# Kernel tuning notes

Measured on AMD Instinct MI355X. Metric: run time of the kernel, lower is better.

Reference implementation:

```python
import jax, jax.numpy as jnp
import numpy as np

GRID_SIZE = 8
SPLINE_ORDER = 3
GRID_LO, GRID_HI = -1.0, 1.0
EPS = 1e-5  # InstanceNorm2d default eps
C = 16
K = GRID_SIZE + SPLINE_ORDER  # number of B-spline basis channels per input channel


def make_grid():
    h = (GRID_HI - GRID_LO) / GRID_SIZE
    # extended knot vector, length grid_size + 2*spline_order + 1
    return jnp.arange(-SPLINE_ORDER, GRID_SIZE + SPLINE_ORDER + 1, dtype=jnp.float32) * h + GRID_LO


def bspline_bases(x, grid):
    # x: [B,C,H,W] -> bases: [B,C,H,W,K] via Cox-de Boor recursion
    xu = x[..., None]
    bases = ((xu >= grid[:-1]) & (xu < grid[1:])).astype(x.dtype)
    for k in range(1, SPLINE_ORDER + 1):
        left = grid[:-(k + 1)]
        right = grid[k:-1]
        delta = jnp.where(right == left, jnp.ones_like(right), right - left)
        bases = ((xu - left) / delta) * bases[..., :-1] + \
                ((grid[k + 1:] - xu) / (grid[k + 1:] - grid[1:-k])) * bases[..., 1:]
    return bases


def conv2d(x, w):
    # NCHW conv, stride 1, padding 1 (kernel 3x3), bias=False as in KANConv2DLayer
    return jax.lax.conv_general_dilated(
        x, w, window_strides=(1, 1), padding=[(1, 1), (1, 1)],
        dimension_numbers=('NCHW', 'OIHW', 'NCHW'))


def instance_norm(x):
    # nn.InstanceNorm2d(affine=False): normalize over H,W per (N,C)
    m = jnp.mean(x, axis=(2, 3), keepdims=True)
    v = jnp.var(x, axis=(2, 3), keepdims=True)
    return (x - m) * jax.lax.rsqrt(v + EPS)


def prelu(x, a):
    return jnp.where(x >= 0, x, a * x)


def kan_conv_layer(x, base_w, spline_w, prelu_a, grid):
    base_out = conv2d(jax.nn.silu(x), base_w)
    b = bspline_bases(x, grid)                      # [B,C,H,W,K]
    B, Cx, H, W, Kx = b.shape
    b = jnp.moveaxis(b, -1, 2).reshape(B, Cx * Kx, H, W)
    spline_out = conv2d(b, spline_w)
    return prelu(instance_norm(base_out + spline_out), prelu_a)


def setup_inputs() -> dict:
    key = jax.random.key(0)
    ks = jax.random.split(key, 5)
    s = 0.05
    return {
        'x': jax.random.normal(ks[0], (4, C, 512, 512), jnp.float32),
        'base_w1': jax.random.normal(ks[1], (C, C, 3, 3), jnp.float32) * s,
        'spline_w1': jax.random.normal(ks[2], (C, C * K, 3, 3), jnp.float32) * s,
        'prelu_a1': jnp.float32(0.25),
        'base_w2': jax.random.normal(ks[3], (C, C, 3, 3), jnp.float32) * s,
        'spline_w2': jax.random.normal(ks[4], (C, C * K, 3, 3), jnp.float32) * s,
        'prelu_a2': jnp.float32(0.25),
    }


def reference(x, base_w1, spline_w1, prelu_a1, base_w2, spline_w2, prelu_a2):
    grid = make_grid()
    y = kan_conv_layer(x, base_w1, spline_w1, prelu_a1, grid)
    y = kan_conv_layer(y, base_w2, spline_w2, prelu_a2, grid)
    return jax.nn.sigmoid(y)
```

## Files before the change

kernel.cpp:

```cpp
#include <hip/hip_runtime.h>
#include <cstddef>
#include <cstdint>

#define HW    512
#define CCH   16
#define TR    12
#define HTILE 18
#define NPIX2 252
#define NSLOT 12

typedef _Float16 f16x8 __attribute__((ext_vector_type(8)));
typedef float    f32x4 __attribute__((ext_vector_type(4)));

__device__ __forceinline__ float h2f(ushort u) {
    _Float16 h = __builtin_bit_cast(_Float16, u);
    return (float)h;
}
__device__ __forceinline__ ushort f2h(float f) {
    _Float16 h = (_Float16)f;
    return __builtin_bit_cast(ushort, h);
}
__device__ __forceinline__ uint pack2h(float a, float b) {
    return (uint)f2h(a) | ((uint)f2h(b) << 16);
}

__device__ __forceinline__ void derived12(float x, uint* u) {
    float si = x / (1.0f + __expf(-x));
    float t  = fmaf(x, 4.0f, 7.0f);
    t = fminf(fmaxf(t, -1.0f), 15.0f);
    float ft = floorf(t);
    int   ci = (int)ft;
    float uu = t - ft;
    float um = 1.0f - uu;
    float u2 = uu * uu, m2 = um * um;
    float u3 = u2 * uu, m3 = m2 * um;
    const float c16 = 0.16666667f, c23 = 0.66666667f;
    float w0 = u3 * c16;
    float w3 = m3 * c16;
    float w2 = fmaf(0.5f, u3, c23 - u2);
    float w1 = fmaf(0.5f, m3, c23 - m2);
    uint64_t P = (uint64_t)f2h(w3)
               | ((uint64_t)f2h(w2) << 16)
               | ((uint64_t)f2h(w1) << 32)
               | ((uint64_t)f2h(w0) << 48);
    int s = 16 * ci - 48;
    int d = s >> 6;
    int e = s & 63;
    uint64_t Q = P << e;
    uint64_t R = (P >> (63 - e)) >> 1;
    uint64_t O0 = (d == 0) ? Q : (d == -1) ? R : 0ull;
    uint64_t O1 = (d == 1) ? Q : (d ==  0) ? R : 0ull;
    uint64_t O2 = (d == 2) ? Q : (d ==  1) ? R : 0ull;
    O2 = (O2 & 0x0000ffffffffffffull) | ((uint64_t)f2h(si) << 48);
    u[0] = (uint)O0; u[1] = (uint)(O0 >> 32);
    u[2] = (uint)O1; u[3] = (uint)(O1 >> 32);
    u[4] = (uint)O2; u[5] = (uint)(O2 >> 32);
}

__global__ void __launch_bounds__(64) prep_w(
    const float* __restrict__ bw1, const float* __restrict__ sw1,
    const float* __restrict__ bw2, const float* __restrict__ sw2,
    uint4* __restrict__ wtab1, uint4* __restrict__ wtab2,
    float* __restrict__ part1, float* __restrict__ part2)
{
    const int s    = blockIdx.x;
    const int lane = threadIdx.x;
    const float* bw; const float* sw; uint4* wt;
    if (blockIdx.y == 0) { bw = bw1; sw = sw1; wt = wtab1; }
    else                 { bw = bw2; sw = sw2; wt = wtab2; }

    if (s == 0) {
        float* p = (blockIdx.y == 0) ? part1 : part2;
        p[lane] = 0.0f;
        p[64 + lane] = 0.0f;
    }

    const int co = lane & 15, q = lane >> 4;
    const int chunk = s / 27, sl = s - chunk * 27;
    uint u[4];
#pragma unroll
    for (int jj = 0; jj < 4; ++jj) {
        float w[2];
#pragma unroll
        for (int h = 0; h < 2; ++h) {
            int j   = jj * 2 + h;
            int kl  = 32 * sl + 8 * q + j;
            int tap = kl / 96;
            int r   = kl - tap * 96;
            int ci  = r / 12;
            int kv  = r - ci * 12;
            int cin = chunk * 8 + ci;
            w[h] = (kv == 11) ? bw[(co * 16 + cin) * 9 + tap]
                              : sw[(co * 176 + cin * 11 + kv) * 9 + tap];
        }
        u[jj] = pack2h(w[0], w[1]);
    }
    wt[s * 64 + lane] = make_uint4(u[0], u[1], u[2], u[3]);
}

template<bool IN_H, bool OUT_H, bool NORM_IN>
__global__ __launch_bounds__(256, 2) void conv_mfma(
    const void* __restrict__ in_v,
    const uint4* __restrict__ wtab,
    void* __restrict__ out_v,
    const float* __restrict__ stats_in,
    const float* __restrict__ a_in,
    float* __restrict__ part_out)
{
    __shared__ uint4 dt16[NSLOT * NPIX2];
    __shared__ float sn[32];

    const int tid  = threadIdx.x;
    const int lane = tid & 63;
    const int wv   = tid >> 6;
    const int m    = lane & 15;
    const int q    = lane >> 4;
    const int bx0  = blockIdx.x * 16;
    const int by0  = blockIdx.y * TR;
    const int b    = blockIdx.z;

    const float*  inf = (const float*)in_v;
    const ushort* inh = (const ushort*)in_v;

    float pa = 0.0f;
    if (NORM_IN) {
        pa = *a_in;
        if (tid < 32) sn[tid] = stats_in[b * 32 + tid];
    }

    f32x4 acc[3];
#pragma unroll
    for (int t = 0; t < 3; ++t) acc[t] = f32x4{0.f, 0.f, 0.f, 0.f};

#pragma unroll 1
    for (int chunk = 0; chunk < 2; ++chunk) {
        __syncthreads();

        float v0[4], v1[4];
        uint  bofs[4], cps[4];
        bool  live[4];
#pragma unroll
        for (int k = 0; k < 4; ++k) {
            int it  = tid + k * 256;
            bool lv = (it < NPIX2 * 4);
            int cp  = it & 3;
            int pix = it >> 2;
            if (!lv) pix = 0;
            int py  = pix / HTILE;
            int px  = pix - py * HTILE;
            int gy  = by0 + py - 1;
            int gx  = bx0 + px - 1;
            bool ok = lv && ((unsigned)gy < (unsigned)HW)
                         && ((unsigned)gx < (unsigned)HW);
            live[k] = lv;
            cps[k]  = (uint)cp;
            bofs[k] = (uint)(cp * 3 * NPIX2 + pix);
            float a = -1.0e9f, c = -1.0e9f;
            if (ok) {
                size_t base = ((size_t)(b * CCH + chunk * 8 + cp * 2) << 18)
                            + ((size_t)gy << 9) + gx;
                if (IN_H) { a = h2f(inh[base]); c = h2f(inh[base + (1u << 18)]); }
                else      { a = inf[base];      c = inf[base + (1u << 18)]; }
            }
            v0[k] = a; v1[k] = c;
        }

        uint4 wf[27];
#pragma unroll
        for (int s = 0; s < 27; ++s) wf[s] = wtab[(chunk * 27 + s) * 64 + lane];

#pragma unroll
        for (int k = 0; k < 4; ++k) {
            if (live[k]) {
                float a0 = v0[k], c0 = v1[k];
                if (NORM_IN) {
                    int ci2 = (chunk * 8 + (int)cps[k] * 2) * 2;
                    a0 = (a0 - sn[ci2])     * sn[ci2 + 1];
                    a0 = (a0 >= 0.f) ? a0 : pa * a0;
                    c0 = (c0 - sn[ci2 + 2]) * sn[ci2 + 3];
                    c0 = (c0 >= 0.f) ? c0 : pa * c0;
                }
                uint uA[6], uB[6];
                derived12(a0, uA);
                derived12(c0, uB);
                uint bo = bofs[k];
                dt16[bo]             = make_uint4(uA[0], uA[1], uA[2], uA[3]);
                dt16[bo + NPIX2]     = make_uint4(uA[4], uA[5], uB[0], uB[1]);
                dt16[bo + 2 * NPIX2] = make_uint4(uB[2], uB[3], uB[4], uB[5]);
            }
        }
        __syncthreads();

        const uint pixbase = (uint)(wv * 3 * HTILE + m);
#pragma unroll
        for (int j = 0; j < 3; ++j) {
            const uint slotoff = (uint)((j * 4 + q) * NPIX2) + pixbase;
#pragma unroll
            for (int tdx = 0; tdx < 3; ++tdx) {
                f16x8 brow[5];
#pragma unroll
                for (int r6 = 0; r6 < 5; ++r6)
                    brow[r6] = *reinterpret_cast<const f16x8*>(
                        &dt16[slotoff + (uint)(r6 * HTILE + tdx)]);
#pragma unroll
                for (int tdy = 0; tdy < 3; ++tdy) {
                    const int s = (tdy * 3 + tdx) * 3 + j;
#pragma unroll
                    for (int t = 0; t < 3; ++t) {
                        acc[t] = __builtin_amdgcn_mfma_f32_16x16x32_f16(
                            __builtin_bit_cast(f16x8, wf[s]), brow[t + tdy],
                            acc[t], 0, 0, 0);
                    }
                }
            }
        }
    }

#pragma unroll
    for (int t = 0; t < 3; ++t) {
        int oy = by0 + wv * 3 + t;
        if (oy < HW) {
#pragma unroll
            for (int r = 0; r < 4; ++r) {
                int co = q * 4 + r;
                size_t idx = ((size_t)(b * CCH + co) << 18)
                           + ((size_t)oy << 9) + (bx0 + m);
                if (OUT_H) ((ushort*)out_v)[idx] = f2h(acc[t][r]);
                else       ((float*)out_v)[idx]  = acc[t][r];
            }
        }
    }

    float s4[4], q4[4];
#pragma unroll
    for (int r = 0; r < 4; ++r) { s4[r] = 0.0f; q4[r] = 0.0f; }
#pragma unroll
    for (int t = 0; t < 3; ++t) {
        int oy = by0 + wv * 3 + t;
        if (oy < HW) {
#pragma unroll
            for (int r = 0; r < 4; ++r) {
                s4[r] += acc[t][r];
                q4[r] = fmaf(acc[t][r], acc[t][r], q4[r]);
            }
        }
    }
#pragma unroll
    for (int off = 8; off > 0; off >>= 1) {
#pragma unroll
        for (int r = 0; r < 4; ++r) {
            s4[r] += __shfl_xor(s4[r], off);
            q4[r] += __shfl_xor(q4[r], off);
        }
    }
    __syncthreads();
    float* scr = (float*)dt16;
    if (m == 0) {
#pragma unroll
        for (int r = 0; r < 4; ++r) {
            scr[(wv * 16 + q * 4 + r) * 2 + 0] = s4[r];
            scr[(wv * 16 + q * 4 + r) * 2 + 1] = q4[r];
        }
    }
    __syncthreads();
    if (tid < 32) {
        int co = tid >> 1, which = tid & 1;
        float v = scr[(0 * 16 + co) * 2 + which] + scr[(1 * 16 + co) * 2 + which]
                + scr[(2 * 16 + co) * 2 + which] + scr[(3 * 16 + co) * 2 + which];
        atomicAdd(&part_out[(size_t)(b * CCH + co) * 2 + which], v);
    }
}

__global__ void __launch_bounds__(64) reduce_final(
    const float* __restrict__ part, float* __restrict__ stats)
{
    const int bc = threadIdx.x;
    const float inv = 1.0f / 262144.0f;
    float s  = part[bc * 2];
    float qq = part[bc * 2 + 1];
    float mval = s * inv;
    float var  = qq * inv - mval * mval;
    stats[bc * 2]     = mval;
    stats[bc * 2 + 1] = rsqrtf(var + 1e-5f);
}

__global__ void __launch_bounds__(256) final_sigmoid(
    float* __restrict__ out, const float* __restrict__ stats,
    const float* __restrict__ a_ptr)
{
    const float a = *a_ptr;
    const int i4 = blockIdx.x * 256 + threadIdx.x;
    const int bc = i4 >> 16;
    const float mm = stats[bc * 2];
    const float rr = stats[bc * 2 + 1];
    float4 v = reinterpret_cast<float4*>(out)[i4];
    float t;
    t = (v.x - mm) * rr; t = (t >= 0.f) ? t : a * t; v.x = 1.0f / (1.0f + __expf(-t));
    t = (v.y - mm) * rr; t = (t >= 0.f) ? t : a * t; v.y = 1.0f / (1.0f + __expf(-t));
    t = (v.z - mm) * rr; t = (t >= 0.f) ? t : a * t; v.z = 1.0f / (1.0f + __expf(-t));
    t = (v.w - mm) * rr; t = (t >= 0.f) ? t : a * t; v.w = 1.0f / (1.0f + __expf(-t));
    reinterpret_cast<float4*>(out)[i4] = v;
}

extern "C" void kernel_launch(void* const* d_in, const int* in_sizes, int n_in,
                              void* d_out, int out_size, void* d_ws, size_t ws_size,
                              hipStream_t stream)
{
    const float* x        = (const float*)d_in[0];
    const float* base_w1  = (const float*)d_in[1];
    const float* spline_w1= (const float*)d_in[2];
    const float* prelu_a1 = (const float*)d_in[3];
    const float* base_w2  = (const float*)d_in[4];
    const float* spline_w2= (const float*)d_in[5];
    const float* prelu_a2 = (const float*)d_in[6];
    float* out_f = (float*)d_out;
    char*  wsb   = (char*)d_ws;

    ushort* z1h    = (ushort*)wsb;
    uint4*  wtab1  = (uint4*)(wsb + 33554432);
    uint4*  wtab2  = (uint4*)(wsb + 33609728);
    float*  part1  = (float*)(wsb + 33665024);
    float*  part2  = (float*)(wsb + 33665536);
    float*  stats1 = (float*)(wsb + 33666048);
    float*  stats2 = (float*)(wsb + 33666560);

    dim3 cgrid(HW / 16, (HW + TR - 1) / TR, 4);
    dim3 cblk(256);

    prep_w<<<dim3(54, 2), 64, 0, stream>>>(base_w1, spline_w1, base_w2, spline_w2,
                                           wtab1, wtab2, part1, part2);

    conv_mfma<false, true, false><<<cgrid, cblk, 0, stream>>>(
        x, wtab1, z1h, nullptr, nullptr, part1);
    reduce_final<<<1, 64, 0, stream>>>(part1, stats1);

    conv_mfma<true, false, true><<<cgrid, cblk, 0, stream>>>(
        z1h, wtab2, out_f, stats1, prelu_a1, part2);
    reduce_final<<<1, 64, 0, stream>>>(part2, stats2);

    final_sigmoid<<<16384, cblk, 0, stream>>>(out_f, stats2, prelu_a2);
}
```

Before: 385.6 us.

## Warp-specialize conv kernel into producer/consumer halves with double-buffered LDS staging

The conv block grows to 512 threads. Four producer waves compute the B-spline/SiLU fp16 features into one of two LDS buffers while four consumer waves run MFMA on the other buffer. Each block now covers two 16-wide column tiles in sequence, and the row stride is padded from 252 to 254 entries, which may reduce LDS bank conflicts. This is meant to overlap feature generation with matrix math. In exchange it doubles LDS use, which may lower occupancy, and adds block-wide barriers between stages.

```diff
diff --git a/kernel.cpp b/kernel.cpp
--- a/kernel.cpp
+++ b/kernel.cpp
@@ -6,8 +6,11 @@
 #define CCH   16
 #define TR    12
 #define HTILE 18
-#define NPIX2 252
+#define HTR   14
+#define NPIXR 252
+#define NPIXP 254
 #define NSLOT 12
+#define BUFU  (NSLOT * NPIXP)
 
 typedef _Float16 f16x8 __attribute__((ext_vector_type(8)));
 typedef float    f32x4 __attribute__((ext_vector_type(4)));
@@ -99,7 +102,7 @@
 }
 
 template<bool IN_H, bool OUT_H, bool NORM_IN>
-__global__ __launch_bounds__(256, 2) void conv_mfma(
+__global__ __launch_bounds__(512, 2) void conv_mfma(
     const void* __restrict__ in_v,
     const uint4* __restrict__ wtab,
     void* __restrict__ out_v,
@@ -107,101 +110,97 @@
     const float* __restrict__ a_in,
     float* __restrict__ part_out)
 {
-    __shared__ uint4 dt16[NSLOT * NPIX2];
-    __shared__ float sn[32];
+    __shared__ uint4 dt16[2][BUFU];
+    __shared__ float scr[128];
 
     const int tid  = threadIdx.x;
+    const bool isC = tid < 256;
     const int lane = tid & 63;
-    const int wv   = tid >> 6;
+    const int wv   = (tid >> 6) & 3;
     const int m    = lane & 15;
     const int q    = lane >> 4;
-    const int bx0  = blockIdx.x * 16;
+    const int ptid = tid & 255;
     const int by0  = blockIdx.y * TR;
+    const int bxA  = blockIdx.x * 32;
+    const int bxB  = bxA + 16;
     const int b    = blockIdx.z;
 
     const float*  inf = (const float*)in_v;
     const ushort* inh = (const ushort*)in_v;
 
     float pa = 0.0f;
-    if (NORM_IN) {
-        pa = *a_in;
-        if (tid < 32) sn[tid] = stats_in[b * 32 + tid];
-    }
+    if (NORM_IN && !isC) pa = *a_in;
 
     f32x4 acc[3];
-#pragma unroll
-    for (int t = 0; t < 3; ++t) acc[t] = f32x4{0.f, 0.f, 0.f, 0.f};
-
-#pragma unroll 1
-    for (int chunk = 0; chunk < 2; ++chunk) {
-        __syncthreads();
-
+
+    auto stage = [&](int bx0t, int c, uint4* __restrict__ buf) {
         float v0[4], v1[4];
-        uint  bofs[4], cps[4];
+        float4 nm[4];
+        uint  bo4[4];
         bool  live[4];
 #pragma unroll
         for (int k = 0; k < 4; ++k) {
-            int it  = tid + k * 256;
-            bool lv = (it < NPIX2 * 4);
+            int it  = ptid + k * 256;
+            bool lv = (it < NPIXR * 4);
             int cp  = it & 3;
             int pix = it >> 2;
             if (!lv) pix = 0;
             int py  = pix / HTILE;
             int px  = pix - py * HTILE;
             int gy  = by0 + py - 1;
-            int gx  = bx0 + px - 1;
+            int gx  = bx0t + px - 1;
             bool ok = lv && ((unsigned)gy < (unsigned)HW)
                          && ((unsigned)gx < (unsigned)HW);
             live[k] = lv;
-            cps[k]  = (uint)cp;
-            bofs[k] = (uint)(cp * 3 * NPIX2 + pix);
-            float a = -1.0e9f, c = -1.0e9f;
+            bo4[k]  = (uint)(cp * 3 * NPIXP + pix);
+            float a = -1.0e9f, cc = -1.0e9f;
             if (ok) {
-                size_t base = ((size_t)(b * CCH + chunk * 8 + cp * 2) << 18)
+                size_t base = ((size_t)(b * CCH + c * 8 + cp * 2) << 18)
                             + ((size_t)gy << 9) + gx;
-                if (IN_H) { a = h2f(inh[base]); c = h2f(inh[base + (1u << 18)]); }
-                else      { a = inf[base];      c = inf[base + (1u << 18)]; }
-            }
-            v0[k] = a; v1[k] = c;
-        }
-
-        uint4 wf[27];
-#pragma unroll
-        for (int s = 0; s < 27; ++s) wf[s] = wtab[(chunk * 27 + s) * 64 + lane];
-
+                if (IN_H) { a = h2f(inh[base]); cc = h2f(inh[base + (1u << 18)]); }
+                else      { a = inf[base];      cc = inf[base + (1u << 18)]; }
+            }
+            if (NORM_IN && lv)
+                nm[k] = *reinterpret_cast<const float4*>(
+                    &stats_in[b * 32 + (c * 8 + cp * 2) * 2]);
+            v0[k] = a; v1[k] = cc;
+        }
 #pragma unroll
         for (int k = 0; k < 4; ++k) {
             if (live[k]) {
                 float a0 = v0[k], c0 = v1[k];
                 if (NORM_IN) {
-                    int ci2 = (chunk * 8 + (int)cps[k] * 2) * 2;
-                    a0 = (a0 - sn[ci2])     * sn[ci2 + 1];
+                    a0 = (a0 - nm[k].x) * nm[k].y;
                     a0 = (a0 >= 0.f) ? a0 : pa * a0;
-                    c0 = (c0 - sn[ci2 + 2]) * sn[ci2 + 3];
+                    c0 = (c0 - nm[k].z) * nm[k].w;
                     c0 = (c0 >= 0.f) ? c0 : pa * c0;
                 }
                 uint uA[6], uB[6];
                 derived12(a0, uA);
                 derived12(c0, uB);
-                uint bo = bofs[k];
-                dt16[bo]             = make_uint4(uA[0], uA[1], uA[2], uA[3]);
-                dt16[bo + NPIX2]     = make_uint4(uA[4], uA[5], uB[0], uB[1]);
-                dt16[bo + 2 * NPIX2] = make_uint4(uB[2], uB[3], uB[4], uB[5]);
-            }
-        }
-        __syncthreads();
-
+                uint bo = bo4[k];
+                buf[bo]             = make_uint4(uA[0], uA[1], uA[2], uA[3]);
+                buf[bo + NPIXP]     = make_uint4(uA[4], uA[5], uB[0], uB[1]);
+                buf[bo + 2 * NPIXP] = make_uint4(uB[2], uB[3], uB[4], uB[5]);
+            }
+        }
+    };
+
+    auto krun = [&](int c, const uint4* __restrict__ buf) {
+        uint4 wf[27];
+#pragma unroll
+        for (int s = 0; s < 27; ++s) wf[s] = wtab[(c * 27 + s) * 64 + lane];
         const uint pixbase = (uint)(wv * 3 * HTILE + m);
 #pragma unroll
         for (int j = 0; j < 3; ++j) {
-            const uint slotoff = (uint)((j * 4 + q) * NPIX2) + pixbase;
+            const uint slotoff = (uint)((j * 4 + q) * NPIXP) + pixbase;
 #pragma unroll
             for (int tdx = 0; tdx < 3; ++tdx) {
                 f16x8 brow[5];
 #pragma unroll
                 for (int r6 = 0; r6 < 5; ++r6)
                     brow[r6] = *reinterpret_cast<const f16x8*>(
-                        &dt16[slotoff + (uint)(r6 * HTILE + tdx)]);
+                        &buf[slotoff + (uint)(r6 * HTILE + tdx)]);
 #pragma unroll
                 for (int tdy = 0; tdy < 3; ++tdy) {
                     const int s = (tdy * 3 + tdx) * 3 + j;
@@ -214,61 +213,83 @@
                 }
             }
         }
-    }
-
-#pragma unroll
-    for (int t = 0; t < 3; ++t) {
-        int oy = by0 + wv * 3 + t;
-        if (oy < HW) {
+    };
+
+    auto epi1 = [&](int bx0t) {
+#pragma unroll
+        for (int t = 0; t < 3; ++t) {
+            int oy = by0 + wv * 3 + t;
+            if (oy < HW) {
+#pragma unroll
+                for (int r = 0; r < 4; ++r) {
+                    int co = q * 4 + r;
+                    size_t idx = ((size_t)(b * CCH + co) << 18)
+                               + ((size_t)oy << 9) + (bx0t + m);
+                    if (OUT_H) ((ushort*)out_v)[idx] = f2h(acc[t][r]);
+                    else       ((float*)out_v)[idx]  = acc[t][r];
+                }
+            }
+        }
+        float s4[4], q4[4];
+#pragma unroll
+        for (int r = 0; r < 4; ++r) { s4[r] = 0.0f; q4[r] = 0.0f; }
+#pragma unroll
+        for (int t = 0; t < 3; ++t) {
+            int oy = by0 + wv * 3 + t;
+            if (oy < HW) {
+#pragma unroll
+                for (int r = 0; r < 4; ++r) {
+                    s4[r] += acc[t][r];
+                    q4[r] = fmaf(acc[t][r], acc[t][r], q4[r]);
+                }
+            }
+        }
+#pragma unroll
+        for (int off = 8; off > 0; off >>= 1) {
 #pragma unroll
             for (int r = 0; r < 4; ++r) {
-                int co = q * 4 + r;
-                size_t idx = ((size_t)(b * CCH + co) << 18)
-                           + ((size_t)oy << 9) + (bx0 + m);
-                if (OUT_H) ((ushort*)out_v)[idx] = f2h(acc[t][r]);
-                else       ((float*)out_v)[idx]  = acc[t][r];
-            }
-        }
-    }
-
-    float s4[4], q4[4];
-#pragma unroll
-    for (int r = 0; r < 4; ++r) { s4[r] = 0.0f; q4[r] = 0.0f; }
-#pragma unroll
-    for (int t = 0; t < 3; ++t) {
-        int oy = by0 + wv * 3 + t;
-        if (oy < HW) {
+                s4[r] += __shfl_xor(s4[r], off);
+                q4[r] += __shfl_xor(q4[r], off);
+            }
+        }
+        if (m == 0) {
 #pragma unroll
             for (int r = 0; r < 4; ++r) {
-                s4[r] += acc[t][r];
-                q4[r] = fmaf(acc[t][r], acc[t][r], q4[r]);
-            }
-        }
-    }
-#pragma unroll
-    for (int off = 8; off > 0; off >>= 1) {
-#pragma unroll
-        for (int r = 0; r < 4; ++r) {
-            s4[r] += __shfl_xor(s4[r], off);
-            q4[r] += __shfl_xor(q4[r], off);
-        }
-    }
-    __syncthreads();
-    float* scr = (float*)dt16;
-    if (m == 0) {
-#pragma unroll
-        for (int r = 0; r < 4; ++r) {
-            scr[(wv * 16 + q * 4 + r) * 2 + 0] = s4[r];
-            scr[(wv * 16 + q * 4 + r) * 2 + 1] = q4[r];
-        }
-    }
-    __syncthreads();
-    if (tid < 32) {
-        int co = tid >> 1, which = tid & 1;
-        float v = scr[(0 * 16 + co) * 2 + which] + scr[(1 * 16 + co) * 2 + which]
-                + scr[(2 * 16 + co) * 2 + which] + scr[(3 * 16 + co) * 2 + which];
-        atomicAdd(&part_out[(size_t)(b * CCH + co) * 2 + which], v);
-    }
+                scr[(wv * 16 + q * 4 + r) * 2 + 0] = s4[r];
+                scr[(wv * 16 + q * 4 + r) * 2 + 1] = q4[r];
+            }
+        }
+    };
+
+    auto epi2 = [&]() {
+        if (tid < 32) {
+            int co = tid >> 1, which = tid & 1;
+            float v = scr[(0 * 16 + co) * 2 + which]
+                    + scr[(1 * 16 + co) * 2 + which]
+                    + scr[(2 * 16 + co) * 2 + which]
+                    + scr[(3 * 16 + co) * 2 + which];
+            atomicAdd(&part_out[(size_t)(b * CCH + co) * 2 + which], v);
+        }
+    };
+
+#define ACCZ do { _Pragma("unroll") \
+    for (int t = 0; t < 3; ++t) acc[t] = f32x4{0.f, 0.f, 0.f, 0.f}; } while (0)
+
+    if (!isC) stage(bxA, 0, dt16[0]);
+    __syncthreads();
+    if (!isC) stage(bxA, 1, dt16[1]);
+    else      { ACCZ; krun(0, dt16[0]); }
+    __syncthreads();
+    if (!isC) stage(bxB, 0, dt16[0]);
+    else      { krun(1, dt16[1]); epi1(bxA); }
+    __syncthreads();
+    if (!isC) stage(bxB, 1, dt16[1]);
+    else      { epi2(); ACCZ; krun(0, dt16[0]); }
+    __syncthreads();
+    if (isC)  { krun(1, dt16[1]); epi1(bxB); }
+    __syncthreads();
+    if (isC)  epi2();
+#undef ACCZ
 }
 
 __global__ void __launch_bounds__(64) reduce_final(
@@ -324,8 +345,9 @@
     float*  stats1 = (float*)(wsb + 33666048);
     float*  stats2 = (float*)(wsb + 33666560);
 
-    dim3 cgrid(HW / 16, (HW + TR - 1) / TR, 4);
-    dim3 cblk(256);
+    dim3 cgrid(HW / 32, (HW + TR - 1) / TR, 4);
+    dim3 cblk(512);
+    dim3 eblk(256);
 
     prep_w<<<dim3(54, 2), 64, 0, stream>>>(base_w1, spline_w1, base_w2, spline_w2,
                                            wtab1, wtab2, part1, part2);
@@ -338,5 +360,5 @@
         z1h, wtab2, out_f, stats1, prelu_a1, part2);
     reduce_final<<<1, 64, 0, stream>>>(part2, stats2);
 
-    final_sigmoid<<<16384, cblk, 0, stream>>>(out_f, stats2, prelu_a2);
-}
+    final_sigmoid<<<16384, eblk, 0, stream>>>(out_f, stats2, prelu_a2);
+}
```

Measured after the change: 478.0 us. 1.24x slower.
